# Kernel tuning notes

Measured on AMD Instinct MI355X. Metric: run time of the kernel, lower is better.

Reference implementation:

```python
import jax, jax.numpy as jnp
import numpy as np

A_MIN = 0.001
EPS = 1e-08


def setup_inputs() -> dict:
    key = jax.random.key(0)
    k1, k2, k3, k4 = jax.random.split(key, 4)
    B, O, I = 512, 1024, 512
    x = jax.random.normal(k1, (B, I), dtype=jnp.float32)
    translation = jax.random.uniform(k2, (O, I), dtype=jnp.float32, minval=-1.0, maxval=1.0)
    scale_raw = jax.random.uniform(k3, (O, I), dtype=jnp.float32, minval=-2.0, maxval=0.0)
    weights = jax.random.normal(k4, (O, I), dtype=jnp.float32) * (1.0 / np.sqrt(I))
    return {"x": x, "translation": translation, "scale_raw": scale_raw, "weights": weights}


def reference(x, translation, scale_raw, weights):
    # x: (B, I); params: (O, I)
    scale = A_MIN + jax.nn.softplus(scale_raw)  # (O, I)
    # s: (B, O, I) broadcast intermediate
    s = (x[:, None, :] - translation[None, :, :]) / (scale[None, :, :] + EPS)
    s2 = s * s
    wavelet = (1.0 - s2) * jnp.exp(-0.5 * s2)  # mexican hat
    y = jnp.einsum('oi,boi->bo', weights, wavelet)  # reduce over in_features
    return y
```

## Files before the change

### kernel.cpp

```cpp
#include <hip/hip_runtime.h>
#include <hip/hip_bf16.h>


#define WL_A_MIN 0.001f
#define WL_EPS   1e-8f

constexpr int WL_B = 512;
constexpr int WL_O = 1024;
constexpr int WL_I = 512;

constexpr int B_TILE = 64;
constexpr int O_TILE = 16;
constexpr int KC     = 64;

constexpr int P_STRIDE = KC * 4 + 4;
constexpr int X_STRIDE = KC + 4;

__device__ __forceinline__ float fast_exp2(float a) {
#if defined(__has_builtin)
#if __has_builtin(__builtin_amdgcn_exp2f)
    return __builtin_amdgcn_exp2f(a);
#else
    return exp2f(a);
#endif
#else
    return exp2f(a);
#endif
}

#define WL_KC (-0.72134752044448170368f)

__global__ __launch_bounds__(256) void wl_precompute(
    const float* __restrict__ translation,
    const float* __restrict__ scale_raw,
    const float* __restrict__ weights,
    float4* __restrict__ ws4)
{
    int idx = blockIdx.x * 256 + threadIdx.x;
    if (idx >= WL_O * WL_I) return;
    float t  = translation[idx];
    float sr = scale_raw[idx];
    float w  = weights[idx];
    float sp  = logf(1.0f + __expf(sr));
    float inv = 1.0f / (WL_A_MIN + sp + WL_EPS);
    ws4[idx] = make_float4(-t * inv, inv, w, 0.0f);
}

__global__ __launch_bounds__(256, 2) void wl_main(
    const float* __restrict__ x,
    const float4* __restrict__ p4,
    float* __restrict__ out)
{
    __shared__ float p_lds[O_TILE * P_STRIDE];
    __shared__ float x_lds[B_TILE * X_STRIDE];

    const int tid    = threadIdx.x;
    const int ox     = tid & 15;
    const int bg     = tid >> 4;
    const int o_base = blockIdx.y * O_TILE;
    const int b_base = blockIdx.x * B_TILE;

    float acc0 = 0.f, acc1 = 0.f, acc2 = 0.f, acc3 = 0.f;

    for (int kc = 0; kc < WL_I; kc += KC) {
        #pragma unroll
        for (int k = 0; k < 4; ++k) {
            int lin = k * 256 + tid;
            int o_l = lin >> 6;
            int i_l = lin & 63;
            float4 v = p4[(o_base + o_l) * WL_I + kc + i_l];
            *reinterpret_cast<float4*>(&p_lds[o_l * P_STRIDE + i_l * 4]) = v;
        }
        #pragma unroll
        for (int k = 0; k < 4; ++k) {
            int lin = k * 256 + tid;
            int b_l = lin >> 4;
            int i4  = lin & 15;
            float4 v = *reinterpret_cast<const float4*>(
                &x[(b_base + b_l) * WL_I + kc + i4 * 4]);
            *reinterpret_cast<float4*>(&x_lds[b_l * X_STRIDE + i4 * 4]) = v;
        }
        __syncthreads();

        const float* xr = &x_lds[(bg * 4) * X_STRIDE];
        const float* pr = &p_lds[ox * P_STRIDE];

        #pragma unroll 8
        for (int i = 0; i < KC; ++i) {
            float4 p = *reinterpret_cast<const float4*>(&pr[i * 4]);
            const float nti = p.x, inv = p.y, w = p.z;
            const float x0 = xr[i];
            const float x1 = xr[X_STRIDE + i];
            const float x2 = xr[2 * X_STRIDE + i];
            const float x3 = xr[3 * X_STRIDE + i];

            {
                float s  = fmaf(x0, inv, nti);
                float s2 = s * s;
                float e  = fast_exp2(s2 * (float)WL_KC);
                float pt = fmaf(-s2, e, e);
                acc0 = fmaf(w, pt, acc0);
            }
            {
                float s  = fmaf(x1, inv, nti);
                float s2 = s * s;
                float e  = fast_exp2(s2 * (float)WL_KC);
                float pt = fmaf(-s2, e, e);
                acc1 = fmaf(w, pt, acc1);
            }
            {
                float s  = fmaf(x2, inv, nti);
                float s2 = s * s;
                float e  = fast_exp2(s2 * (float)WL_KC);
                float pt = fmaf(-s2, e, e);
                acc2 = fmaf(w, pt, acc2);
            }
            {
                float s  = fmaf(x3, inv, nti);
                float s2 = s * s;
                float e  = fast_exp2(s2 * (float)WL_KC);
                float pt = fmaf(-s2, e, e);
                acc3 = fmaf(w, pt, acc3);
            }
        }
        __syncthreads();
    }

    const int o  = o_base + ox;
    const int b0 = b_base + bg * 4;
    out[(b0 + 0) * WL_O + o] = acc0;
    out[(b0 + 1) * WL_O + o] = acc1;
    out[(b0 + 2) * WL_O + o] = acc2;
    out[(b0 + 3) * WL_O + o] = acc3;
}

extern "C" void kernel_launch(void* const* d_in, const int* in_sizes, int n_in,
                              void* d_out, int out_size, void* d_ws, size_t ws_size,
                              hipStream_t stream) {
    const float* x           = (const float*)d_in[0];
    const float* translation = (const float*)d_in[1];
    const float* scale_raw   = (const float*)d_in[2];
    const float* weights     = (const float*)d_in[3];
    float*       out         = (float*)d_out;
    float4*      ws4         = (float4*)d_ws;

    wl_precompute<<<dim3((WL_O * WL_I + 255) / 256), dim3(256), 0, stream>>>(
        translation, scale_raw, weights, ws4);

    wl_main<<<dim3(WL_B / B_TILE, WL_O / O_TILE), dim3(256), 0, stream>>>(
        x, ws4, out);
}
```

Before: 122.5 us.

## Fuse parameter precompute into main kernel with packed-FP32 math and transposed x tile

Drops the separate precompute kernel and its float4 workspace, and computes softplus scale, inverse and weight terms on the fly while each tile loads into LDS. The batch tile shrinks from 64 to 32 with two batch rows per thread, and the x tile is stored transposed so a thread reads both rows with one v2f load. Scaling constants are folded into inv and w so the inner loop uses a bare exp2 and packed-FP32 FMAs. In exchange, the transcendental parameter work is repeated for every batch tile (16 times instead of once), which adds per-tile exp, log and rcp cost.

```diff
diff --git a/kernel.cpp b/kernel.cpp
--- a/kernel.cpp
+++ b/kernel.cpp
@@ -9,58 +9,60 @@
 constexpr int WL_O = 1024;
 constexpr int WL_I = 512;
 
-constexpr int B_TILE = 64;
 constexpr int O_TILE = 16;
+constexpr int B_TILE = 32;
 constexpr int KC     = 64;
 
-constexpr int P_STRIDE = KC * 4 + 4;
-constexpr int X_STRIDE = KC + 4;
+constexpr int PS = KC * 4 + 4;
+constexpr int XS = B_TILE + 4;
+
+#define WL_K    0.72134752044448170368f
+#define WL_SQK  0.84932180553704583800f
+#define WL_IK   1.38629436111989061883f
+#define WL_L2E  1.44269504088896340736f
+#define WL_LN2  0.69314718055994530942f
+
+typedef float v2f __attribute__((ext_vector_type(2)));
 
 __device__ __forceinline__ float fast_exp2(float a) {
-#if defined(__has_builtin)
 #if __has_builtin(__builtin_amdgcn_exp2f)
     return __builtin_amdgcn_exp2f(a);
 #else
     return exp2f(a);
 #endif
+}
+__device__ __forceinline__ float fast_log2(float a) {
+#if __has_builtin(__builtin_amdgcn_logf)
+    return __builtin_amdgcn_logf(a);
 #else
-    return exp2f(a);
+    return __log2f(a);
+#endif
+}
+__device__ __forceinline__ float fast_rcp(float a) {
+#if __has_builtin(__builtin_amdgcn_rcpf)
+    return __builtin_amdgcn_rcpf(a);
+#else
+    return 1.0f / a;
 #endif
 }
 
-#define WL_KC (-0.72134752044448170368f)
-
-__global__ __launch_bounds__(256) void wl_precompute(
+__global__ __launch_bounds__(256, 4) void wl_fused(
+    const float* __restrict__ x,
     const float* __restrict__ translation,
     const float* __restrict__ scale_raw,
     const float* __restrict__ weights,
-    float4* __restrict__ ws4)
-{
-    int idx = blockIdx.x * 256 + threadIdx.x;
-    if (idx >= WL_O * WL_I) return;
-    float t  = translation[idx];
-    float sr = scale_raw[idx];
-    float w  = weights[idx];
-    float sp  = logf(1.0f + __expf(sr));
-    float inv = 1.0f / (WL_A_MIN + sp + WL_EPS);
-    ws4[idx] = make_float4(-t * inv, inv, w, 0.0f);
-}
-
-__global__ __launch_bounds__(256, 2) void wl_main(
-    const float* __restrict__ x,
-    const float4* __restrict__ p4,
     float* __restrict__ out)
 {
-    __shared__ float p_lds[O_TILE * P_STRIDE];
-    __shared__ float x_lds[B_TILE * X_STRIDE];
+    __shared__ float p_lds[O_TILE * PS];
+    __shared__ float x_lds[KC * XS];
 
     const int tid    = threadIdx.x;
     const int ox     = tid & 15;
     const int bg     = tid >> 4;
-    const int o_base = blockIdx.y * O_TILE;
-    const int b_base = blockIdx.x * B_TILE;
+    const int o_base = blockIdx.x * O_TILE;
+    const int b_base = blockIdx.y * B_TILE;
 
-    float acc0 = 0.f, acc1 = 0.f, acc2 = 0.f, acc3 = 0.f;
+    v2f acc = {0.0f, 0.0f};
 
     for (int kc = 0; kc < WL_I; kc += KC) {
         #pragma unroll
@@ -68,70 +70,60 @@
             int lin = k * 256 + tid;
             int o_l = lin >> 6;
             int i_l = lin & 63;
-            float4 v = p4[(o_base + o_l) * WL_I + kc + i_l];
-            *reinterpret_cast<float4*>(&p_lds[o_l * P_STRIDE + i_l * 4]) = v;
+            int gi  = (o_base + o_l) * WL_I + kc + i_l;
+            float t  = translation[gi];
+            float sr = scale_raw[gi];
+            float w  = weights[gi];
+            float ex  = fast_exp2(sr * WL_L2E);
+            float sp  = fast_log2(1.0f + ex) * WL_LN2;
+            float inv = fast_rcp(WL_A_MIN + sp + WL_EPS);
+            float inv_s = inv * WL_SQK;
+            float4 pv = make_float4(-t * inv_s, inv_s, w, w * WL_IK);
+            *reinterpret_cast<float4*>(&p_lds[o_l * PS + i_l * 4]) = pv;
         }
-        #pragma unroll
-        for (int k = 0; k < 4; ++k) {
-            int lin = k * 256 + tid;
-            int b_l = lin >> 4;
-            int i4  = lin & 15;
-            float4 v = *reinterpret_cast<const float4*>(
-                &x[(b_base + b_l) * WL_I + kc + i4 * 4]);
-            *reinterpret_cast<float4*>(&x_lds[b_l * X_STRIDE + i4 * 4]) = v;
+        {
+            int b_r = tid & 31;
+            int ig  = tid >> 5;
+            const float4* xr = reinterpret_cast<const float4*>(
+                &x[(b_base + b_r) * WL_I + kc + ig * 8]);
+            float4 v0 = xr[0];
+            float4 v1 = xr[1];
+            int base = (ig * 8) * XS + b_r;
+            x_lds[base + 0 * XS] = v0.x;
+            x_lds[base + 1 * XS] = v0.y;
+            x_lds[base + 2 * XS] = v0.z;
+            x_lds[base + 3 * XS] = v0.w;
+            x_lds[base + 4 * XS] = v1.x;
+            x_lds[base + 5 * XS] = v1.y;
+            x_lds[base + 6 * XS] = v1.z;
+            x_lds[base + 7 * XS] = v1.w;
         }
         __syncthreads();
 
-        const float* xr = &x_lds[(bg * 4) * X_STRIDE];
-        const float* pr = &p_lds[ox * P_STRIDE];
+        const float* pr = &p_lds[ox * PS];
 
         #pragma unroll 8
         for (int i = 0; i < KC; ++i) {
             float4 p = *reinterpret_cast<const float4*>(&pr[i * 4]);
-            const float nti = p.x, inv = p.y, w = p.z;
-            const float x0 = xr[i];
-            const float x1 = xr[X_STRIDE + i];
-            const float x2 = xr[2 * X_STRIDE + i];
-            const float x3 = xr[3 * X_STRIDE + i];
-
-            {
-                float s  = fmaf(x0, inv, nti);
-                float s2 = s * s;
-                float e  = fast_exp2(s2 * (float)WL_KC);
-                float pt = fmaf(-s2, e, e);
-                acc0 = fmaf(w, pt, acc0);
-            }
-            {
-                float s  = fmaf(x1, inv, nti);
-                float s2 = s * s;
-                float e  = fast_exp2(s2 * (float)WL_KC);
-                float pt = fmaf(-s2, e, e);
-                acc1 = fmaf(w, pt, acc1);
-            }
-            {
-                float s  = fmaf(x2, inv, nti);
-                float s2 = s * s;
-                float e  = fast_exp2(s2 * (float)WL_KC);
-                float pt = fmaf(-s2, e, e);
-                acc2 = fmaf(w, pt, acc2);
-            }
-            {
-                float s  = fmaf(x3, inv, nti);
-                float s2 = s * s;
-                float e  = fast_exp2(s2 * (float)WL_KC);
-                float pt = fmaf(-s2, e, e);
-                acc3 = fmaf(w, pt, acc3);
-            }
+            v2f x2 = *reinterpret_cast<const v2f*>(&x_lds[i * XS + bg * 2]);
+            v2f inv2 = {p.y, p.y};
+            v2f nti2 = {p.x, p.x};
+            v2f s  = __builtin_elementwise_fma(x2, inv2, nti2);
+            v2f u  = s * s;
+            v2f e  = {fast_exp2(-u.x), fast_exp2(-u.y)};
+            v2f w2  = {p.z, p.z};
+            acc = __builtin_elementwise_fma(w2, e, acc);
+            v2f ue = u * e;
+            v2f nw2 = {-p.w, -p.w};
+            acc = __builtin_elementwise_fma(nw2, ue, acc);
         }
         __syncthreads();
     }
 
-    const int o  = o_base + ox;
-    const int b0 = b_base + bg * 4;
-    out[(b0 + 0) * WL_O + o] = acc0;
-    out[(b0 + 1) * WL_O + o] = acc1;
-    out[(b0 + 2) * WL_O + o] = acc2;
-    out[(b0 + 3) * WL_O + o] = acc3;
+    const int o = o_base + ox;
+    const int b = b_base + bg * 2;
+    out[(b + 0) * WL_O + o] = acc.x;
+    out[(b + 1) * WL_O + o] = acc.y;
 }
 
 extern "C" void kernel_launch(void* const* d_in, const int* in_sizes, int n_in,
@@ -142,11 +134,7 @@
     const float* scale_raw   = (const float*)d_in[2];
     const float* weights     = (const float*)d_in[3];
     float*       out         = (float*)d_out;
-    float4*      ws4         = (float4*)d_ws;
 
-    wl_precompute<<<dim3((WL_O * WL_I + 255) / 256), dim3(256), 0, stream>>>(
-        translation, scale_raw, weights, ws4);
-
-    wl_main<<<dim3(WL_B / B_TILE, WL_O / O_TILE), dim3(256), 0, stream>>>(
-        x, ws4, out);
+    wl_fused<<<dim3(WL_O / O_TILE, WL_B / B_TILE), dim3(256), 0, stream>>>(
+        x, translation, scale_raw, weights, out);
 }
```

Measured after the change: 113.4 us. -7.4%, faster.
